# Kernel optimization log

Measured on AMD Instinct MI355X. Metric: run time of the kernel, lower is better.

Reference implementation:

```python
import jax, jax.numpy as jnp
import numpy as np

B, S, D = 16, 2048, 128

def setup_inputs() -> dict:
    key = jax.random.key(0)
    kq, kk, kv = jax.random.split(key, 3)
    Q = jax.random.normal(kq, (B, S, D), dtype=jnp.float32)
    K = jax.random.normal(kk, (B, S, D), dtype=jnp.float32)
    V = jax.random.normal(kv, (B, S, D), dtype=jnp.float32)
    mask = jnp.ones((B, S), dtype=jnp.int32)  # key padding mask; 0 = masked out
    return {"Q": Q, "K": K, "V": V, "mask": mask}

def reference(Q, K, V, mask):
    scale = jnp.asarray(D ** 0.5, dtype=Q.dtype)
    # scores: [B, Sq, Sk]
    scores = jnp.einsum('bqd,bkd->bqk', Q, K) / scale
    neg_inf = jnp.asarray(float('-inf'), dtype=scores.dtype)
    # mask==0 -> -inf, broadcast over query dim: [B, 1, Sk]
    scores = jnp.where((mask == 0)[:, None, :], neg_inf, scores)
    attn = jax.nn.softmax(scores, axis=-1)
    out = jnp.einsum('bqk,bkd->bqd', attn, V)
    return (out, attn)
```

## Files before the change

### kernel.cpp

```cpp
#include <hip/hip_runtime.h>

#define BB 16
#define SS 2048
#define DD 128
#define SCALE 0.08838834764831845f

typedef __attribute__((ext_vector_type(8))) short bf16x8;
typedef __attribute__((ext_vector_type(4))) float f32x4;

__device__ __forceinline__ unsigned short f2bf(float f) {
    union { float f; unsigned int u; } v; v.f = f;
    unsigned int u = v.u;
    return (unsigned short)((u + 0x7fffu + ((u >> 16) & 1u)) >> 16);
}

__device__ __forceinline__ void gload16(const void* g, void* l) {
    __builtin_amdgcn_global_load_lds((const __attribute__((address_space(1))) void*)g,
                                     (__attribute__((address_space(3))) void*)l, 16, 0, 0);
}

__global__ __launch_bounds__(256) void cvt_bf16_kernel(const float* __restrict__ src,
                                                       unsigned short* __restrict__ dst) {
    int idx = (blockIdx.x * 256 + threadIdx.x) * 4;
    float4 f = *(const float4*)(src + idx);
    ushort4 o;
    o.x = f2bf(f.x); o.y = f2bf(f.y); o.z = f2bf(f.z); o.w = f2bf(f.w);
    *(ushort4*)(dst + idx) = o;
}

__global__ __launch_bounds__(256) void transpose_v_kernel(const float* __restrict__ v,
                                                          unsigned short* __restrict__ vt) {
    __shared__ unsigned short sT[64 * 132];
    int b = blockIdx.x >> 5;
    int s0 = (blockIdx.x & 31) * 64;
    int tid = threadIdx.x;
#pragma unroll
    for (int rnd = 0; rnd < 8; ++rnd) {
        int slot = rnd * 256 + tid;
        int row = slot >> 5;
        int c4 = (slot & 31) * 4;
        float4 f = *(const float4*)(v + (size_t)(b * SS + s0 + row) * DD + c4);
        unsigned short* p = &sT[row * 132 + c4];
        p[0] = f2bf(f.x); p[1] = f2bf(f.y); p[2] = f2bf(f.z); p[3] = f2bf(f.w);
    }
    __syncthreads();
#pragma unroll
    for (int rnd = 0; rnd < 4; ++rnd) {
        int slot = rnd * 256 + tid;
        int d = slot >> 3;
        int k8 = (slot & 7) * 8;
        __align__(16) unsigned short tmp[8];
#pragma unroll
        for (int e = 0; e < 8; ++e) tmp[e] = sT[(k8 + e) * 132 + d];
        *(ushort4*)(vt + (size_t)(b * DD + d) * SS + s0 + k8) = *(ushort4*)&tmp[0];
        *(ushort4*)(vt + (size_t)(b * DD + d) * SS + s0 + k8 + 4) = *(ushort4*)&tmp[4];
    }
}

__global__ __launch_bounds__(256) void attn_kernel(const unsigned short* __restrict__ Qb,
                                                   const unsigned short* __restrict__ Kb,
                                                   const unsigned short* __restrict__ Vt,
                                                   const int* __restrict__ mask,
                                                   float* __restrict__ outO,
                                                   float* __restrict__ outA) {
    __shared__ unsigned short sA[64 * 128];
    __shared__ unsigned short sB[64 * 128];
    __shared__ unsigned short sC[64 * 128];
    __shared__ unsigned short sQ[64 * 136];
    __shared__ unsigned short sP[64 * 72];
    __shared__ float sLpart[2][64];
    __shared__ float sLinv[64];

    int bi = blockIdx.x;
    int slot = bi >> 3;
    int b = (bi & 7) * 2 + (slot >> 5);
    int qt = slot & 31;

    int tid = threadIdx.x;
    int wave = tid >> 6, lane = tid & 63, lo = lane & 15, hi = lane >> 4;
    const int sw = lo & 7;

    const int kq0 = (wave >> 1) * 32;
    const int qq0 = (wave & 1) * 32;
    const int dv0 = wave * 32;

    const unsigned short* Qbase = Qb + (size_t)(b * SS + qt * 64) * DD;
#pragma unroll
    for (int rnd = 0; rnd < 4; ++rnd) {
        int sl = rnd * 256 + tid;
        int row = sl >> 4, coff = (sl & 15) * 8;
        *(int4*)&sQ[row * 136 + coff] = *(const int4*)(Qbase + row * DD + coff);
    }

    const char* KB = (const char*)(Kb + (size_t)b * SS * DD);
    const char* VB = (const char*)(Vt + (size_t)b * DD * SS);
    const int* maskB = mask + (size_t)b * SS;

    const int RK = wave * 4 + (lane >> 4);
    const unsigned CK = (unsigned)(RK * 256 + (((lane & 15) ^ (RK & 7)) << 4));
    const unsigned CV = (unsigned)(wave * 32768 + (lane >> 3) * 4096 +
                                   (((lane & 7) ^ (lane >> 3)) << 4));

    auto ISSUE_K = [&](int kt, unsigned short* dst) {
        const char* src = KB + (size_t)kt * 16384 + CK;
        char* d = (char*)dst + wave * 1024;
#pragma unroll
        for (int i = 0; i < 4; ++i)
            gload16(src + i * 4096, d + i * 4096);
    };
    auto ISSUE_V = [&](int kt, unsigned short* dst) {
        const char* src = VB + (size_t)kt * 128 + CV;
        char* d = (char*)dst + wave * 1024;
#pragma unroll
        for (int i = 0; i < 4; ++i)
            gload16(src + (size_t)i * 131072, d + i * 4096);
    };

    auto QK = [&](const unsigned short* kb, f32x4 (&acc)[2][2]) {
#pragma unroll
        for (int ii = 0; ii < 2; ++ii)
#pragma unroll
            for (int jj = 0; jj < 2; ++jj) acc[ii][jj] = (f32x4){0.f, 0.f, 0.f, 0.f};
        __builtin_amdgcn_s_setprio(1);
#pragma unroll
        for (int ks = 0; ks < 4; ++ks) {
            bf16x8 af[2], bfr[2];
#pragma unroll
            for (int ii = 0; ii < 2; ++ii) {
                int row = kq0 + ii * 16 + lo;
                int ch = (ks * 4 + hi) ^ sw;
                af[ii] = *(const bf16x8*)((const char*)kb + row * 256 + (ch << 4));
            }
#pragma unroll
            for (int jj = 0; jj < 2; ++jj)
                bfr[jj] = *(const bf16x8*)&sQ[(qq0 + jj * 16 + lo) * 136 + ks * 32 + hi * 8];
#pragma unroll
            for (int ii = 0; ii < 2; ++ii)
#pragma unroll
                for (int jj = 0; jj < 2; ++jj)
                    acc[ii][jj] = __builtin_amdgcn_mfma_f32_16x16x32_bf16(af[ii], bfr[jj], acc[ii][jj], 0, 0, 0);
        }
        __builtin_amdgcn_s_setprio(0);
    };

    float lsum0 = 0.f, lsum1 = 0.f;

    ISSUE_K(0, sA);
#pragma unroll 1
    for (int t = 0; t < 32; ++t) {
        __syncthreads();
        if (t < 31) ISSUE_K(t + 1, (t & 1) ? sA : sB);
        f32x4 acc[2][2];
        QK((t & 1) ? sB : sA, acc);
        int4 w0 = *(const int4*)(maskB + t * 64 + kq0 + hi * 4);
        int4 w1 = *(const int4*)(maskB + t * 64 + kq0 + 16 + hi * 4);
        float m0[4] = {w0.x ? 1.f : 0.f, w0.y ? 1.f : 0.f, w0.z ? 1.f : 0.f, w0.w ? 1.f : 0.f};
        float m1[4] = {w1.x ? 1.f : 0.f, w1.y ? 1.f : 0.f, w1.z ? 1.f : 0.f, w1.w ? 1.f : 0.f};
#pragma unroll
        for (int r = 0; r < 4; ++r) {
            lsum0 += __expf(acc[0][0][r] * SCALE) * m0[r] + __expf(acc[1][0][r] * SCALE) * m1[r];
            lsum1 += __expf(acc[0][1][r] * SCALE) * m0[r] + __expf(acc[1][1][r] * SCALE) * m1[r];
        }
    }

    {
        float v0 = lsum0, v1 = lsum1;
        v0 += __shfl_xor(v0, 16); v0 += __shfl_xor(v0, 32);
        v1 += __shfl_xor(v1, 16); v1 += __shfl_xor(v1, 32);
        if (lane < 16) {
            sLpart[kq0 >> 5][qq0 + lane] = v0;
            sLpart[kq0 >> 5][qq0 + 16 + lane] = v1;
        }
    }
    __syncthreads();
    if (tid < 64) sLinv[tid] = 1.f / (sLpart[0][tid] + sLpart[1][tid]);
    __syncthreads();
    const float linv0 = sLinv[qq0 + lo];
    const float linv1 = sLinv[qq0 + 16 + lo];

    f32x4 oacc[2][4];
#pragma unroll
    for (int tj = 0; tj < 2; ++tj)
#pragma unroll
        for (int mi = 0; mi < 4; ++mi) oacc[tj][mi] = (f32x4){0.f, 0.f, 0.f, 0.f};

    float* Abase = outA + (size_t)(b * SS + qt * 64) * SS;

    ISSUE_K(0, sA);
    ISSUE_V(0, sB);
#pragma unroll 1
    for (int t = 0; t < 32; ++t) {
        unsigned short* vcur = (t & 1) ? sC : sB;
        __syncthreads();
        if (t < 31) ISSUE_V(t + 1, (t & 1) ? sB : sC);
        f32x4 acc[2][2];
        QK(sA, acc);
        int4 w0 = *(const int4*)(maskB + t * 64 + kq0 + hi * 4);
        int4 w1 = *(const int4*)(maskB + t * 64 + kq0 + 16 + hi * 4);
        float m0[4] = {w0.x ? 1.f : 0.f, w0.y ? 1.f : 0.f, w0.z ? 1.f : 0.f, w0.w ? 1.f : 0.f};
        float m1[4] = {w1.x ? 1.f : 0.f, w1.y ? 1.f : 0.f, w1.z ? 1.f : 0.f, w1.w ? 1.f : 0.f};
#pragma unroll
        for (int jj = 0; jj < 2; ++jj) {
            int q = qq0 + jj * 16 + lo;
            float li = jj ? linv1 : linv0;
#pragma unroll
            for (int ii = 0; ii < 2; ++ii) {
                f32x4 p;
#pragma unroll
                for (int r = 0; r < 4; ++r) {
                    float mv = ii ? m1[r] : m0[r];
                    p[r] = __expf(acc[ii][jj][r] * SCALE) * mv * li;
                }
                int kcol = kq0 + ii * 16 + hi * 4;
                *(f32x4*)(Abase + (size_t)q * SS + t * 64 + kcol) = p;
                ushort4 pb;
                pb.x = f2bf(p[0]); pb.y = f2bf(p[1]); pb.z = f2bf(p[2]); pb.w = f2bf(p[3]);
                *(ushort4*)&sP[q * 72 + kcol] = pb;
            }
        }
        __syncthreads();
        if (t < 31) ISSUE_K(t + 1, sA);
        __builtin_amdgcn_s_setprio(1);
#pragma unroll
        for (int ks = 0; ks < 2; ++ks) {
            bf16x8 pa[4], vb[2];
#pragma unroll
            for (int mi = 0; mi < 4; ++mi)
                pa[mi] = *(const bf16x8*)&sP[(mi * 16 + lo) * 72 + ks * 32 + hi * 8];
#pragma unroll
            for (int tj = 0; tj < 2; ++tj) {
                int rowv = dv0 + tj * 16 + lo;
                int ch = (ks * 4 + hi) ^ sw;
                vb[tj] = *(const bf16x8*)((const char*)vcur + rowv * 128 + (ch << 4));
            }
#pragma unroll
            for (int tj = 0; tj < 2; ++tj)
#pragma unroll
                for (int mi = 0; mi < 4; ++mi)
                    oacc[tj][mi] = __builtin_amdgcn_mfma_f32_16x16x32_bf16(vb[tj], pa[mi], oacc[tj][mi], 0, 0, 0);
        }
        __builtin_amdgcn_s_setprio(0);
    }

    float* Obase = outO + (size_t)(b * SS + qt * 64) * DD;
#pragma unroll
    for (int tj = 0; tj < 2; ++tj) {
#pragma unroll
        for (int mi = 0; mi < 4; ++mi) {
            int q = mi * 16 + lo;
            int dv = dv0 + tj * 16 + hi * 4;
            *(f32x4*)(Obase + (size_t)q * DD + dv) = oacc[tj][mi];
        }
    }
}

extern "C" void kernel_launch(void* const* d_in, const int* in_sizes, int n_in,
                              void* d_out, int out_size, void* d_ws, size_t ws_size,
                              hipStream_t stream) {
    const float* Q = (const float*)d_in[0];
    const float* K = (const float*)d_in[1];
    const float* V = (const float*)d_in[2];
    const int* mask = (const int*)d_in[3];

    float* outO = (float*)d_out;
    float* outA = outO + (size_t)BB * SS * DD;

    unsigned short* Qb = (unsigned short*)d_ws;
    unsigned short* Kb = Qb + (size_t)BB * SS * DD;
    unsigned short* Vt = Kb + (size_t)BB * SS * DD;

    int nconv = (BB * SS * DD) / (256 * 4);
    cvt_bf16_kernel<<<nconv, 256, 0, stream>>>(Q, Qb);
    cvt_bf16_kernel<<<nconv, 256, 0, stream>>>(K, Kb);
    transpose_v_kernel<<<BB * (SS / 64), 256, 0, stream>>>(V, Vt);
    attn_kernel<<<BB * (SS / 64), 256, 0, stream>>>(Qb, Kb, Vt, mask, outO, outA);
}
```

Baseline: 389.1 us.

## Keep Q in registers, double-buffer K and V, and use explicit waitcnt barriers

Q fragments are now loaded once into registers, which removes the Q shared-memory tile and its per-step LDS reads. The freed LDS holds a fourth buffer, so the second pass double-buffers both K and V and prefetches the next K and V tiles together at the top of each iteration. The old version reloaded K mid-iteration after a second barrier. The __syncthreads calls are replaced by explicit vmcnt/lgkmcnt waits plus raw s_barrier and sched_barrier, and the mask loads are hoisted ahead of the QK MMA. This adds register pressure from the 8 held Q fragments, and correctness now depends on the hand-placed waitcnt ordering.

```diff
diff --git a/kernel.cpp b/kernel.cpp
--- a/kernel.cpp
+++ b/kernel.cpp
@@ -7,6 +7,11 @@
 
 typedef __attribute__((ext_vector_type(8))) short bf16x8;
 typedef __attribute__((ext_vector_type(4))) float f32x4;
+
+#define WAIT_VM0()   asm volatile("s_waitcnt vmcnt(0)" ::: "memory")
+#define WAIT_LGKM0() asm volatile("s_waitcnt lgkmcnt(0)" ::: "memory")
+#define BAR()        __builtin_amdgcn_s_barrier()
+#define SCHED0()     __builtin_amdgcn_sched_barrier(0)
 
 __device__ __forceinline__ unsigned short f2bf(float f) {
     union { float f; unsigned int u; } v; v.f = f;
@@ -66,7 +71,7 @@
     __shared__ unsigned short sA[64 * 128];
     __shared__ unsigned short sB[64 * 128];
     __shared__ unsigned short sC[64 * 128];
-    __shared__ unsigned short sQ[64 * 136];
+    __shared__ unsigned short sD[64 * 128];
     __shared__ unsigned short sP[64 * 72];
     __shared__ float sLpart[2][64];
     __shared__ float sLinv[64];
@@ -85,12 +90,12 @@
     const int dv0 = wave * 32;
 
     const unsigned short* Qbase = Qb + (size_t)(b * SS + qt * 64) * DD;
-#pragma unroll
-    for (int rnd = 0; rnd < 4; ++rnd) {
-        int sl = rnd * 256 + tid;
-        int row = sl >> 4, coff = (sl & 15) * 8;
-        *(int4*)&sQ[row * 136 + coff] = *(const int4*)(Qbase + row * DD + coff);
-    }
+    bf16x8 qf[2][4];
+#pragma unroll
+    for (int jj = 0; jj < 2; ++jj)
+#pragma unroll
+        for (int ks = 0; ks < 4; ++ks)
+            qf[jj][ks] = *(const bf16x8*)(Qbase + (qq0 + jj * 16 + lo) * DD + ks * 32 + hi * 8);
 
     const char* KB = (const char*)(Kb + (size_t)b * SS * DD);
     const char* VB = (const char*)(Vt + (size_t)b * DD * SS);
@@ -124,7 +129,7 @@
         __builtin_amdgcn_s_setprio(1);
 #pragma unroll
         for (int ks = 0; ks < 4; ++ks) {
-            bf16x8 af[2], bfr[2];
+            bf16x8 af[2];
 #pragma unroll
             for (int ii = 0; ii < 2; ++ii) {
                 int row = kq0 + ii * 16 + lo;
@@ -132,13 +137,10 @@
                 af[ii] = *(const bf16x8*)((const char*)kb + row * 256 + (ch << 4));
             }
 #pragma unroll
-            for (int jj = 0; jj < 2; ++jj)
-                bfr[jj] = *(const bf16x8*)&sQ[(qq0 + jj * 16 + lo) * 136 + ks * 32 + hi * 8];
-#pragma unroll
             for (int ii = 0; ii < 2; ++ii)
 #pragma unroll
                 for (int jj = 0; jj < 2; ++jj)
-                    acc[ii][jj] = __builtin_amdgcn_mfma_f32_16x16x32_bf16(af[ii], bfr[jj], acc[ii][jj], 0, 0, 0);
+                    acc[ii][jj] = __builtin_amdgcn_mfma_f32_16x16x32_bf16(af[ii], qf[jj][ks], acc[ii][jj], 0, 0, 0);
         }
         __builtin_amdgcn_s_setprio(0);
     };
@@ -148,12 +150,13 @@
     ISSUE_K(0, sA);
 #pragma unroll 1
     for (int t = 0; t < 32; ++t) {
-        __syncthreads();
+        WAIT_VM0();
+        BAR(); SCHED0();
         if (t < 31) ISSUE_K(t + 1, (t & 1) ? sA : sB);
+        int4 w0 = *(const int4*)(maskB + t * 64 + kq0 + hi * 4);
+        int4 w1 = *(const int4*)(maskB + t * 64 + kq0 + 16 + hi * 4);
         f32x4 acc[2][2];
         QK((t & 1) ? sB : sA, acc);
-        int4 w0 = *(const int4*)(maskB + t * 64 + kq0 + hi * 4);
-        int4 w1 = *(const int4*)(maskB + t * 64 + kq0 + 16 + hi * 4);
         float m0[4] = {w0.x ? 1.f : 0.f, w0.y ? 1.f : 0.f, w0.z ? 1.f : 0.f, w0.w ? 1.f : 0.f};
         float m1[4] = {w1.x ? 1.f : 0.f, w1.y ? 1.f : 0.f, w1.z ? 1.f : 0.f, w1.w ? 1.f : 0.f};
 #pragma unroll
@@ -172,6 +175,8 @@
             sLpart[kq0 >> 5][qq0 + 16 + lane] = v1;
         }
     }
+    ISSUE_K(0, sA);
+    ISSUE_V(0, sC);
     __syncthreads();
     if (tid < 64) sLinv[tid] = 1.f / (sLpart[0][tid] + sLpart[1][tid]);
     __syncthreads();
@@ -186,17 +191,18 @@
 
     float* Abase = outA + (size_t)(b * SS + qt * 64) * SS;
 
-    ISSUE_K(0, sA);
-    ISSUE_V(0, sB);
 #pragma unroll 1
     for (int t = 0; t < 32; ++t) {
-        unsigned short* vcur = (t & 1) ? sC : sB;
-        __syncthreads();
-        if (t < 31) ISSUE_V(t + 1, (t & 1) ? sB : sC);
-        f32x4 acc[2][2];
-        QK(sA, acc);
+        WAIT_VM0();
+        BAR(); SCHED0();
+        if (t < 31) {
+            ISSUE_K(t + 1, (t & 1) ? sA : sB);
+            ISSUE_V(t + 1, (t & 1) ? sC : sD);
+        }
         int4 w0 = *(const int4*)(maskB + t * 64 + kq0 + hi * 4);
         int4 w1 = *(const int4*)(maskB + t * 64 + kq0 + 16 + hi * 4);
+        f32x4 acc[2][2];
+        QK((t & 1) ? sB : sA, acc);
         float m0[4] = {w0.x ? 1.f : 0.f, w0.y ? 1.f : 0.f, w0.z ? 1.f : 0.f, w0.w ? 1.f : 0.f};
         float m1[4] = {w1.x ? 1.f : 0.f, w1.y ? 1.f : 0.f, w1.z ? 1.f : 0.f, w1.w ? 1.f : 0.f};
 #pragma unroll
@@ -218,8 +224,9 @@
                 *(ushort4*)&sP[q * 72 + kcol] = pb;
             }
         }
-        __syncthreads();
-        if (t < 31) ISSUE_K(t + 1, sA);
+        WAIT_LGKM0();
+        BAR(); SCHED0();
+        const unsigned short* vcur = (t & 1) ? sD : sC;
         __builtin_amdgcn_s_setprio(1);
 #pragma unroll
         for (int ks = 0; ks < 2; ++ks) {
```

Measured after the change: 394.3 us. About the same (+1.3%).
